# Kernel optimization log

Hardware: AMD Instinct MI355X
Metric: run time of the kernel (lower is better)

The kernel has to match this reference:

```python
import jax, jax.numpy as jnp
import numpy as np

L, B, T, C, H, FC = 8, 4, 2048, 1024, 16, 4
HD = C // H  # head dim = 64
DFF = FC * C  # 4096


def _layernorm(x, g, b, eps=1e-5):
    mu = jnp.mean(x, axis=-1, keepdims=True)
    var = jnp.mean(jnp.square(x - mu), axis=-1, keepdims=True)
    return (x - mu) * jax.lax.rsqrt(var + eps) * g + b


def setup_inputs() -> dict:
    key = jax.random.key(0)
    ks = jax.random.split(key, 18)
    s = 0.02
    d = {}
    d["x"] = jax.random.normal(ks[0], (B, T, C), jnp.float32)
    d["ln1_g"] = jnp.ones((L, C), jnp.float32)
    d["ln1_b"] = jnp.zeros((L, C), jnp.float32)
    d["ln2_g"] = jnp.ones((L, C), jnp.float32)
    d["ln2_b"] = jnp.zeros((L, C), jnp.float32)
    d["wq"] = jax.random.normal(ks[1], (L, C, C), jnp.float32) * s
    d["bq"] = jnp.zeros((L, C), jnp.float32)
    d["wk"] = jax.random.normal(ks[2], (L, C, C), jnp.float32) * s
    d["bk"] = jnp.zeros((L, C), jnp.float32)
    d["wv"] = jax.random.normal(ks[3], (L, C, C), jnp.float32) * s
    d["bv"] = jnp.zeros((L, C), jnp.float32)
    d["wo"] = jax.random.normal(ks[4], (L, C, C), jnp.float32) * s
    d["bo"] = jnp.zeros((L, C), jnp.float32)
    d["w1"] = jax.random.normal(ks[5], (L, C, DFF), jnp.float32) * s
    d["b1"] = jnp.zeros((L, DFF), jnp.float32)
    d["w2"] = jax.random.normal(ks[6], (L, DFF, C), jnp.float32) * s
    d["b2"] = jnp.zeros((L, C), jnp.float32)
    return d


def _forward(x, ln1_g, ln1_b, ln2_g, ln2_b, wq, bq, wk, bk, wv, bv, wo, bo, w1, b1, w2, b2):
    mask = jnp.tril(jnp.ones((T, T), dtype=bool))  # causal mask (block_size buffer)
    scale = 1.0 / np.sqrt(HD).astype(np.float32)

    def block(h, p):
        g1, be1, g2, be2, Wq, Bq, Wk, Bk, Wv, Bv, Wo, Bo, W1, B1, W2, B2 = p
        hn = _layernorm(h, g1, be1)
        # heads: [B, H, T, HD]
        q = (hn @ Wq + Bq).reshape(B, T, H, HD).transpose(0, 2, 1, 3)
        k = (hn @ Wk + Bk).reshape(B, T, H, HD).transpose(0, 2, 1, 3)
        v = (hn @ Wv + Bv).reshape(B, T, H, HD).transpose(0, 2, 1, 3)
        att = jnp.einsum('bhid,bhjd->bhij', q, k) * scale
        att = jnp.where(mask, att, -jnp.inf)
        att = jax.nn.softmax(att, axis=-1)
        y = jnp.einsum('bhij,bhjd->bhid', att, v)
        y = y.transpose(0, 2, 1, 3).reshape(B, T, C) @ Wo + Bo
        h = h + y
        m = _layernorm(h, g2, be2)
        h = h + jax.nn.gelu(m @ W1 + B1, approximate=False) @ W2 + B2
        return h, None

    params = (ln1_g, ln1_b, ln2_g, ln2_b, wq, bq, wk, bk, wv, bv, wo, bo, w1, b1, w2, b2)
    x, _ = jax.lax.scan(block, x, params)
    return x


def reference(x, ln1_g, ln1_b, ln2_g, ln2_b, wq, bq, wk, bk, wv, bv, wo, bo, w1, b1, w2, b2):
    return _forward(x, ln1_g, ln1_b, ln2_g, ln2_b, wq, bq, wk, bk, wv, bv, wo, bo, w1, b1, w2, b2)
```

## Files before the change

kernel.cpp:

```cpp
#include <hip/hip_runtime.h>
#include <hip/hip_bf16.h>

#define LL 8
#define BBx 4
#define TT 2048
#define CC 1024
#define HH 16
#define HDD 64
#define DFFx 4096
#define MMx 8192

typedef __bf16 bf16;
typedef __attribute__((ext_vector_type(8))) __bf16 bf16x8;
typedef __attribute__((ext_vector_type(4))) __bf16 bf16x4;
typedef __attribute__((ext_vector_type(4))) float f32x4;
typedef __attribute__((ext_vector_type(8))) unsigned short u16x8;

#define QSCALE 0.18033688f

__device__ __forceinline__ unsigned short bfbits(float v) {
  return __builtin_bit_cast(unsigned short, (__bf16)v);
}

__device__ __forceinline__ float fexp2(float x) {
#if __has_builtin(__builtin_amdgcn_exp2f)
  return __builtin_amdgcn_exp2f(x);
#else
  float r;
  asm volatile("v_exp_f32 %0, %1\n\ts_nop 0" : "=v"(r) : "v"(x));
  return r;
#endif
}

__device__ __forceinline__ int xcd_swz(int id, int nwg) {
  return (id & 7) * (nwg >> 3) + (id >> 3);
}

#define GLDS(gp, lp) __builtin_amdgcn_global_load_lds( \
    (const __attribute__((address_space(1))) void*)(gp), \
    (__attribute__((address_space(3))) void*)(lp), 16, 0, 0)

__global__ __launch_bounds__(256) void transpose_cast(
    const float* __restrict__ W, bf16* __restrict__ Wt,
    int K, int N, long srcStride, long dstStride)
{
  __shared__ float tile[32][33];
  const float* Wl = W + (size_t)blockIdx.z * srcStride;
  bf16* Wtl = Wt + (size_t)blockIdx.z * dstStride;
  const int n0 = blockIdx.x * 32, k0 = blockIdx.y * 32;
  const int tx = threadIdx.x, ty = threadIdx.y;
#pragma unroll
  for (int i = 0; i < 32; i += 8)
    tile[ty + i][tx] = Wl[(size_t)(k0 + ty + i) * N + n0 + tx];
  __syncthreads();
#pragma unroll
  for (int i = 0; i < 32; i += 8)
    Wtl[(size_t)(n0 + ty + i) * K + k0 + tx] = (bf16)tile[tx][ty + i];
}

__global__ __launch_bounds__(256) void ln_cmb(
    float* __restrict__ h, const float* __restrict__ p0, const float* __restrict__ p1,
    const float* __restrict__ gamma, const float* __restrict__ beta,
    bf16* __restrict__ out)
{
  const int row = blockIdx.x, tid = threadIdx.x;
  const size_t base = (size_t)row * CC + tid * 4;
  float4 v = *(const float4*)(h + base);
  if (p0) {
    const float4 a = *(const float4*)(p0 + base);
    const float4 b = *(const float4*)(p1 + base);
    v.x += a.x + b.x; v.y += a.y + b.y; v.z += a.z + b.z; v.w += a.w + b.w;
    *(float4*)(h + base) = v;
  }
  if (!out) return;
  float s  = v.x + v.y + v.z + v.w;
  float ss = v.x * v.x + v.y * v.y + v.z * v.z + v.w * v.w;
#pragma unroll
  for (int o = 32; o >= 1; o >>= 1) {
    s  += __shfl_xor(s, o);
    ss += __shfl_xor(ss, o);
  }
  __shared__ float rs[4], rss[4];
  const int w = tid >> 6, l = tid & 63;
  if (l == 0) { rs[w] = s; rss[w] = ss; }
  __syncthreads();
  s  = rs[0] + rs[1] + rs[2] + rs[3];
  ss = rss[0] + rss[1] + rss[2] + rss[3];
  const float mu = s * (1.f / CC);
  const float rstd = rsqrtf(ss * (1.f / CC) - mu * mu + 1e-5f);
  const float4 g  = *(const float4*)(gamma + tid * 4);
  const float4 be = *(const float4*)(beta + tid * 4);
  bf16x4 o4;
  o4[0] = (bf16)((v.x - mu) * rstd * g.x + be.x);
  o4[1] = (bf16)((v.y - mu) * rstd * g.y + be.y);
  o4[2] = (bf16)((v.z - mu) * rstd * g.z + be.z);
  o4[3] = (bf16)((v.w - mu) * rstd * g.w + be.w);
  *(bf16x4*)(out + (size_t)row * CC + tid * 4) = o4;
}

template<int EPI>
__global__ __launch_bounds__(256, 4) void gemm128(
    const bf16* __restrict__ A, const bf16* __restrict__ Bt,
    const float* __restrict__ bias0, const float* __restrict__ bias1,
    const float* __restrict__ bias2,
    bf16* __restrict__ o0, bf16* __restrict__ o1, bf16* __restrict__ o2,
    float* __restrict__ p0, float* __restrict__ p1,
    int M, int N, int K, int lda)
{
  __shared__ __align__(16) bf16 sA[128 * 64];
  __shared__ __align__(16) bf16 sB[128 * 64];
  const int nx = N >> 7;
  int wk = xcd_swz((int)blockIdx.x, (int)gridDim.x);
  int koff = 0;
  float* part = p0;
  bool addb = true;
  if constexpr (EPI == 1) {
    const int tiles = nx * (M >> 7);
    const int ks = wk / tiles;
    wk -= ks * tiles;
    koff = ks * K;
    addb = (ks == 0);
    part = ks ? p1 : p0;
  }
  const int m0 = (wk / nx) * 128;
  const int n0 = (wk % nx) * 128;
  const int tid = threadIdx.x;
  const int w = tid >> 6, l = tid & 63;
  const int wr = w >> 1, wc = w & 1;
  const int lr = l & 15, lk = l >> 4;

  f32x4 acc[4][4] = {};
  const int NT = K >> 6;

  for (int kt = 0; kt < NT; ++kt) {
#pragma unroll
    for (int i = 0; i < 4; ++i) {
      const int e = (tid << 4) + (i << 12);
      const int ro = e >> 7, co = (e & 127) >> 1;
      GLDS(A + (size_t)(m0 + ro) * lda + kt * 64 + koff + co, sA + (e >> 1));
      GLDS(Bt + (size_t)(n0 + ro) * lda + kt * 64 + koff + co, sB + (e >> 1));
    }
    __syncthreads();
#pragma unroll
    for (int kk = 0; kk < 2; ++kk) {
      bf16x8 af[4], bfr[4];
#pragma unroll
      for (int i = 0; i < 4; ++i)
        af[i] = *(const bf16x8*)&sA[(wr * 64 + i * 16 + lr) * 64 + kk * 32 + lk * 8];
#pragma unroll
      for (int j = 0; j < 4; ++j)
        bfr[j] = *(const bf16x8*)&sB[(wc * 64 + j * 16 + lr) * 64 + kk * 32 + lk * 8];
#pragma unroll
      for (int i = 0; i < 4; ++i)
#pragma unroll
        for (int j = 0; j < 4; ++j)
          acc[i][j] = __builtin_amdgcn_mfma_f32_16x16x32_bf16(af[i], bfr[j], acc[i][j], 0, 0, 0);
    }
    __syncthreads();
  }

  if constexpr (EPI == 0) {
    const int seg = n0 >> 10;
    const float* bp = (seg == 0) ? bias0 : (seg == 1 ? bias1 : bias2);
    if (seg < 2) {
      const float qs = (seg == 0) ? QSCALE : 1.0f;
      float bv4[4];
#pragma unroll
      for (int j = 0; j < 4; ++j) bv4[j] = bp[(n0 + wc * 64 + j * 16 + lr) & 1023];
      const int hh = ((n0 + wc * 64) & 1023) >> 6;
      bf16* dst = (seg == 0) ? o0 : o1;
#pragma unroll
      for (int i = 0; i < 4; ++i) {
        const int mrow = m0 + wr * 64 + i * 16 + lk * 4;
        const int bidx = mrow >> 11, t = mrow & 2047;
#pragma unroll
        for (int r = 0; r < 4; ++r) {
          bf16* rowp = dst + (((size_t)(bidx * HH + hh)) * TT + t + r) * HDD;
#pragma unroll
          for (int j = 0; j < 4; ++j)
            rowp[j * 16 + lr] = (bf16)((acc[i][j][r] + bv4[j]) * qs);
        }
      }
    } else {
      char* scb = (w < 2) ? ((char*)sA + w * 8192) : ((char*)sB + (w - 2) * 8192);
#pragma unroll
      for (int j = 0; j < 4; ++j) {
        const int dl = j * 16 + lr;
        const float bv = bias2[(n0 + wc * 64 + dl) & 1023];
#pragma unroll
        for (int i = 0; i < 4; ++i) {
          ushort4 pk;
          pk.x = bfbits(acc[i][j][0] + bv);
          pk.y = bfbits(acc[i][j][1] + bv);
          pk.z = bfbits(acc[i][j][2] + bv);
          pk.w = bfbits(acc[i][j][3] + bv);
          *(ushort4*)(scb + dl * 128 + (((i * 16 + lk * 4) * 2) ^ ((dl & 7) << 4))) = pk;
        }
      }
      asm volatile("s_waitcnt lgkmcnt(0)" ::: "memory");
      const int hh = ((n0 + wc * 64) & 1023) >> 6;
      const int bidx = (m0 + wr * 64) >> 11;
      const int tb = (m0 + wr * 64) & 2047;
      const int c = l & 7;
#pragma unroll
      for (int g = 0; g < 8; ++g) {
        const int dl = g * 8 + (l >> 3);
        u16x8 val = *(const u16x8*)(scb + dl * 128 + ((c * 16) ^ ((dl & 7) << 4)));
        *(u16x8*)&o2[(((size_t)(bidx * HH + hh)) * HDD + dl) * TT + tb + c * 8] = val;
      }
    }
  } else if constexpr (EPI == 1) {
    float bv4[4];
#pragma unroll
    for (int j = 0; j < 4; ++j)
      bv4[j] = addb ? bias0[n0 + wc * 64 + j * 16 + lr] : 0.f;
#pragma unroll
    for (int i = 0; i < 4; ++i) {
      const int mrow = m0 + wr * 64 + i * 16 + lk * 4;
#pragma unroll
      for (int r = 0; r < 4; ++r) {
        float* rowp = part + (size_t)(mrow + r) * N + n0 + wc * 64;
#pragma unroll
        for (int j = 0; j < 4; ++j)
          rowp[j * 16 + lr] = acc[i][j][r] + bv4[j];
      }
    }
  } else {
    float bv4[4];
#pragma unroll
    for (int j = 0; j < 4; ++j) bv4[j] = bias0[n0 + wc * 64 + j * 16 + lr];
#pragma unroll
    for (int i = 0; i < 4; ++i) {
      const int mrow = m0 + wr * 64 + i * 16 + lk * 4;
#pragma unroll
      for (int r = 0; r < 4; ++r) {
        bf16* rowp = o0 + (size_t)(mrow + r) * N + n0 + wc * 64;
#pragma unroll
        for (int j = 0; j < 4; ++j) {
          const float x = acc[i][j][r] + bv4[j];
          rowp[j * 16 + lr] = (bf16)(0.5f * x * (1.f + erff(x * 0.70710678f)));
        }
      }
    }
  }
  (void)M;
}

__global__ __launch_bounds__(256) void attn_fwd(
    const bf16* __restrict__ Q, const bf16* __restrict__ Kk,
    const bf16* __restrict__ Vt, bf16* __restrict__ O)
{
  const int wk = xcd_swz((int)blockIdx.x, (int)gridDim.x);
  const int bh = wk >> 3;
  const int xt = wk & 7;
  const int tid = threadIdx.x;
  const int w = tid >> 6, l = tid & 63;
  const int lr = l & 15, lk = l >> 4;
  const int bidx = bh >> 4, hh = bh & 15;

  const bf16* Qp = Q  + (size_t)bh * (TT * HDD);
  const bf16* Kp = Kk + (size_t)bh * (TT * HDD);
  const bf16* Vp = Vt + (size_t)bh * (HDD * TT);

  __shared__ __align__(16) bf16 sK[64 * 64];
  __shared__ __align__(16) bf16 sV[64 * 64];
  __shared__ __align__(16) bf16 sP[4][16 * 64];
  bf16* sPw = &sP[w][0];

  const int swz = (lr & 7) * 8;
  const int srow = tid >> 3;
  const int scol = (((tid & 7) ^ (srow & 7)) << 3);
  const int sdst = tid << 3;

  for (int half = 0; half < 2; ++half) {
    const int qtile = (half == 0) ? xt : (15 - xt);
    const int q0 = qtile * 128;

    bf16x8 qf[2][2];
#pragma unroll
    for (int qi = 0; qi < 2; ++qi)
#pragma unroll
      for (int dk = 0; dk < 2; ++dk)
        qf[qi][dk] = *(const bf16x8*)&Qp[(size_t)(q0 + w * 32 + qi * 16 + lr) * HDD + dk * 32 + lk * 8];

    f32x4 accO[2][4] = {};
    float mrun[2] = {-__builtin_inff(), -__builtin_inff()};
    float lrun[2] = {0.f, 0.f};
    const int wqmax = q0 + w * 32 + 31;
    const int kvend = q0 + 128;

    for (int kv = 0; kv < kvend; kv += 64) {
      __syncthreads();
#pragma unroll
      for (int i = 0; i < 2; ++i) {
        GLDS(Kp + (size_t)(kv + srow + i * 32) * HDD + scol, sK + sdst + i * 2048);
        GLDS(Vp + (size_t)(srow + i * 32) * TT + kv + scol, sV + sdst + i * 2048);
      }
      __syncthreads();

      if (kv <= wqmax) {
#pragma unroll
        for (int qi = 0; qi < 2; ++qi) {
          f32x4 st[4];
#pragma unroll
          for (int kt = 0; kt < 4; ++kt) {
            f32x4 z = {0.f, 0.f, 0.f, 0.f};
#pragma unroll
            for (int dk = 0; dk < 2; ++dk) {
              bf16x8 kf = *(const bf16x8*)&sK[(kt * 16 + lr) * 64 + ((dk * 32 + lk * 8) ^ swz)];
              z = __builtin_amdgcn_mfma_f32_16x16x32_bf16(kf, qf[qi][dk], z, 0, 0, 0);
            }
            st[kt] = z;
          }
          const int qabs_base = q0 + w * 32 + qi * 16;
          float pm = -__builtin_inff();
          if (kv + 63 > qabs_base) {
            const int qabs = qabs_base + lr;
#pragma unroll
            for (int kt = 0; kt < 4; ++kt)
#pragma unroll
              for (int r = 0; r < 4; ++r) {
                const int kvabs = kv + kt * 16 + lk * 4 + r;
                float val = (kvabs > qabs) ? -__builtin_inff() : st[kt][r];
                st[kt][r] = val;
                pm = fmaxf(pm, val);
              }
          } else {
#pragma unroll
            for (int kt = 0; kt < 4; ++kt)
#pragma unroll
              for (int r = 0; r < 4; ++r) pm = fmaxf(pm, st[kt][r]);
          }
          pm = fmaxf(pm, __shfl_xor(pm, 16));
          pm = fmaxf(pm, __shfl_xor(pm, 32));
          const float mnew = fmaxf(mrun[qi], pm);
          const float alpha = fexp2(mrun[qi] - mnew);
          mrun[qi] = mnew;
          float psum = 0.f;
#pragma unroll
          for (int kt = 0; kt < 4; ++kt) {
            const float p0v = fexp2(st[kt][0] - mnew);
            const float p1v = fexp2(st[kt][1] - mnew);
            const float p2v = fexp2(st[kt][2] - mnew);
            const float p3v = fexp2(st[kt][3] - mnew);
            psum += p0v + p1v + p2v + p3v;
            ushort4 pk;
            pk.x = bfbits(p0v); pk.y = bfbits(p1v); pk.z = bfbits(p2v); pk.w = bfbits(p3v);
            *(ushort4*)&sPw[lr * 64 + ((kt * 16 + lk * 4) ^ swz)] = pk;
          }
          psum += __shfl_xor(psum, 16);
          psum += __shfl_xor(psum, 32);
          lrun[qi] = lrun[qi] * alpha + psum;
          f32x4 al4;
#pragma unroll
          for (int r = 0; r < 4; ++r) al4[r] = __shfl(alpha, lk * 4 + r);
#pragma unroll
          for (int dj = 0; dj < 4; ++dj) accO[qi][dj] *= al4;
#pragma unroll
          for (int kt2 = 0; kt2 < 2; ++kt2) {
            bf16x8 pf = *(const bf16x8*)&sPw[lr * 64 + ((kt2 * 32 + lk * 8) ^ swz)];
#pragma unroll
            for (int dj = 0; dj < 4; ++dj) {
              bf16x8 vf = *(const bf16x8*)&sV[(dj * 16 + lr) * 64 + ((kt2 * 32 + lk * 8) ^ swz)];
              accO[qi][dj] = __builtin_amdgcn_mfma_f32_16x16x32_bf16(pf, vf, accO[qi][dj], 0, 0, 0);
            }
          }
        }
      }
    }

#pragma unroll
    for (int qi = 0; qi < 2; ++qi) {
      const float linv = 1.f / lrun[qi];
      f32x4 li4;
#pragma unroll
      for (int r = 0; r < 4; ++r) li4[r] = __shfl(linv, lk * 4 + r);
      const int tbase = q0 + w * 32 + qi * 16 + lk * 4;
#pragma unroll
      for (int dj = 0; dj < 4; ++dj)
#pragma unroll
        for (int r = 0; r < 4; ++r)
          O[((size_t)bidx * TT + tbase + r) * CC + hh * 64 + dj * 16 + lr] =
              (bf16)(accO[qi][dj][r] * li4[r]);
    }
  }
}

extern "C" void kernel_launch(void* const* d_in, const int* in_sizes, int n_in,
                              void* d_out, int out_size, void* d_ws, size_t ws_size,
                              hipStream_t stream)
{
  const float* x    = (const float*)d_in[0];
  const float* ln1g = (const float*)d_in[1];
  const float* ln1b = (const float*)d_in[2];
  const float* ln2g = (const float*)d_in[3];
  const float* ln2b = (const float*)d_in[4];
  const float* wq   = (const float*)d_in[5];
  const float* bq   = (const float*)d_in[6];
  const float* wk   = (const float*)d_in[7];
  const float* bk   = (const float*)d_in[8];
  const float* wv   = (const float*)d_in[9];
  const float* bvv  = (const float*)d_in[10];
  const float* wo   = (const float*)d_in[11];
  const float* bo   = (const float*)d_in[12];
  const float* w1   = (const float*)d_in[13];
  const float* b1   = (const float*)d_in[14];
  const float* w2   = (const float*)d_in[15];
  const float* b2   = (const float*)d_in[16];

  float* h = (float*)d_out;
  bf16* ws = (bf16*)d_ws;
  bf16* wqkvT = ws;
  bf16* woT   = wqkvT + (size_t)LL * 3 * CC * CC;
  bf16* w1T   = woT + (size_t)LL * CC * CC;
  bf16* w2T   = w1T + (size_t)LL * CC * DFFx;
  bf16* hn    = w2T + (size_t)LL * CC * DFFx;
  bf16* qb    = hn + (size_t)MMx * CC;
  bf16* kb    = qb + (size_t)MMx * CC;
  bf16* vt    = kb + (size_t)MMx * CC;
  bf16* ab    = vt + (size_t)MMx * CC;
  bf16* mid   = ab + (size_t)MMx * CC;

  float* pw0 = (float*)mid;
  float* pw1 = (float*)mid + (size_t)MMx * CC;
  float* pm0 = (float*)qb;
  float* pm1 = (float*)vt;

  hipMemcpyAsync(h, x, (size_t)MMx * CC * sizeof(float), hipMemcpyDeviceToDevice, stream);

  dim3 tb(32, 8);
  transpose_cast<<<dim3(CC / 32, CC / 32, LL), tb, 0, stream>>>(wq, wqkvT, CC, CC, (long)CC * CC, (long)3 * CC * CC);
  transpose_cast<<<dim3(CC / 32, CC / 32, LL), tb, 0, stream>>>(wk, wqkvT + CC * CC, CC, CC, (long)CC * CC, (long)3 * CC * CC);
  transpose_cast<<<dim3(CC / 32, CC / 32, LL), tb, 0, stream>>>(wv, wqkvT + 2 * CC * CC, CC, CC, (long)CC * CC, (long)3 * CC * CC);
  transpose_cast<<<dim3(CC / 32, CC / 32, LL), tb, 0, stream>>>(wo, woT, CC, CC, (long)CC * CC, (long)CC * CC);
  transpose_cast<<<dim3(DFFx / 32, CC / 32, LL), tb, 0, stream>>>(w1, w1T, CC, DFFx, (long)CC * DFFx, (long)CC * DFFx);
  transpose_cast<<<dim3(CC / 32, DFFx / 32, LL), tb, 0, stream>>>(w2, w2T, DFFx, CC, (long)CC * DFFx, (long)CC * DFFx);

  for (int li = 0; li < LL; ++li) {
    if (li == 0)
      ln_cmb<<<MMx, 256, 0, stream>>>(h, nullptr, nullptr, ln1g, ln1b, hn);
    else
      ln_cmb<<<MMx, 256, 0, stream>>>(h, pm0, pm1, ln1g + li * CC, ln1b + li * CC, hn);
    gemm128<0><<<(3 * CC / 128) * (MMx / 128), 256, 0, stream>>>(
        hn, wqkvT + (size_t)li * 3 * CC * CC, bq + li * CC, bk + li * CC, bvv + li * CC,
        qb, kb, vt, nullptr, nullptr, MMx, 3 * CC, CC, CC);
    attn_fwd<<<8 * BBx * HH, 256, 0, stream>>>(qb, kb, vt, ab);
    gemm128<1><<<2 * (CC / 128) * (MMx / 128), 256, 0, stream>>>(
        ab, woT + (size_t)li * CC * CC, bo + li * CC, nullptr, nullptr,
        nullptr, nullptr, nullptr, pw0, pw1, MMx, CC, CC / 2, CC);
    ln_cmb<<<MMx, 256, 0, stream>>>(h, pw0, pw1, ln2g + li * CC, ln2b + li * CC, hn);
    gemm128<2><<<(DFFx / 128) * (MMx / 128), 256, 0, stream>>>(
        hn, w1T + (size_t)li * CC * DFFx, b1 + li * DFFx, nullptr, nullptr,
        mid, nullptr, nullptr, nullptr, nullptr, MMx, DFFx, CC, CC);
    gemm128<1><<<2 * (CC / 128) * (MMx / 128), 256, 0, stream>>>(
        mid, w2T + (size_t)li * CC * DFFx, b2 + li * CC, nullptr, nullptr,
        nullptr, nullptr, nullptr, pm0, pm1, MMx, CC, DFFx / 2, DFFx);
  }
  ln_cmb<<<MMx, 256, 0, stream>>>(h, pm0, pm1, nullptr, nullptr, nullptr);
  (void)in_sizes; (void)n_in; (void)out_size; (void)ws_size;
}
```

Baseline: 3.272 ms.

## Add 256x256 double-buffered GEMM kernel for QKV, FFN1 and FFN2

Adds a gemm256 kernel with 512 threads, 256x256 output tiles, double-buffered LDS staging interleaved with MFMA phases, swizzled LDS layout, and setprio around MFMA bursts. QKV, FFN-up and FFN-down GEMMs switch to it, while gemm128 is trimmed to the split-K fp32 epilogue used for the output projection. The larger tiles are meant to raise arithmetic intensity and hide global-load latency. In exchange the kernel uses more LDS and registers (lower occupancy) and launches fewer blocks, which can leave CUs underused for the N=1024 split-K GEMM.

```diff
diff --git a/kernel.cpp b/kernel.cpp
--- a/kernel.cpp
+++ b/kernel.cpp
@@ -101,9 +101,7 @@
 template<int EPI>
 __global__ __launch_bounds__(256, 4) void gemm128(
     const bf16* __restrict__ A, const bf16* __restrict__ Bt,
-    const float* __restrict__ bias0, const float* __restrict__ bias1,
-    const float* __restrict__ bias2,
-    bf16* __restrict__ o0, bf16* __restrict__ o1, bf16* __restrict__ o2,
+    const float* __restrict__ bias0,
     float* __restrict__ p0, float* __restrict__ p1,
     int M, int N, int K, int lda)
 {
@@ -158,6 +156,120 @@
     }
     __syncthreads();
   }
+  float bv4[4];
+#pragma unroll
+  for (int j = 0; j < 4; ++j)
+    bv4[j] = addb ? bias0[n0 + wc * 64 + j * 16 + lr] : 0.f;
+#pragma unroll
+  for (int i = 0; i < 4; ++i) {
+    const int mrow = m0 + wr * 64 + i * 16 + lk * 4;
+#pragma unroll
+    for (int r = 0; r < 4; ++r) {
+      float* rowp = part + (size_t)(mrow + r) * N + n0 + wc * 64;
+#pragma unroll
+      for (int j = 0; j < 4; ++j)
+        rowp[j * 16 + lr] = acc[i][j][r] + bv4[j];
+    }
+  }
+  (void)M;
+}
+
+template<int EPI>
+__global__ __launch_bounds__(512, 2) void gemm256(
+    const bf16* __restrict__ A, const bf16* __restrict__ Bt,
+    const float* __restrict__ bias0, const float* __restrict__ bias1,
+    const float* __restrict__ bias2,
+    bf16* __restrict__ o0, bf16* __restrict__ o1, bf16* __restrict__ o2,
+    float* __restrict__ p0w, float* __restrict__ p1w,
+    int M, int N, int K, int lda)
+{
+  __shared__ __align__(16) bf16 sA[2][256 * 64];
+  __shared__ __align__(16) bf16 sB[2][256 * 64];
+  const int nx = N >> 8;
+  int wk = xcd_swz((int)blockIdx.x, (int)gridDim.x);
+  int koff = 0;
+  float* part = p0w;
+  bool addb = true;
+  if constexpr (EPI == 1) {
+    const int tiles = nx * (M >> 8);
+    const int ks = wk / tiles;
+    wk -= ks * tiles;
+    koff = ks * K;
+    addb = (ks == 0);
+    part = ks ? p1w : p0w;
+  }
+  const int m0 = (wk / nx) * 256;
+  const int n0 = (wk % nx) * 256;
+  const int tid = threadIdx.x;
+  const int w = tid >> 6, l = tid & 63;
+  const int wm = w >> 2, wn = w & 3;
+  const int lr = l & 15, lk = l >> 4;
+  const int sr = tid >> 3, ss = tid & 7;
+  const int gcs = (ss ^ (sr & 7)) << 3;
+
+  f32x4 acc[8][4] = {};
+  const int NT = K >> 6;
+
+  auto stageq = [&](int b, int kt, int q) {
+    const int gc = gcs + kt * 64 + koff;
+    const int rb = (q & 1) * 128;
+    if (q < 2) {
+#pragma unroll
+      for (int i = 0; i < 2; ++i) {
+        const int r = rb + sr + i * 64;
+        GLDS(A + (size_t)(m0 + r) * lda + gc, &sA[b][r * 64 + ss * 8]);
+      }
+    } else {
+#pragma unroll
+      for (int i = 0; i < 2; ++i) {
+        const int r = rb + sr + i * 64;
+        GLDS(Bt + (size_t)(n0 + r) * lda + gc, &sB[b][r * 64 + ss * 8]);
+      }
+    }
+  };
+
+  stageq(0, 0, 0); stageq(0, 0, 1); stageq(0, 0, 2); stageq(0, 0, 3);
+  asm volatile("s_waitcnt vmcnt(2)" ::: "memory");
+  __builtin_amdgcn_s_barrier();
+
+  bf16x8 af[8], bf2[2];
+  for (int t = 0; t < NT; ++t) {
+    const int cur = t & 1, nxt = cur ^ 1;
+    const bool pre = (t + 1 < NT);
+#pragma unroll
+    for (int ph = 0; ph < 4; ++ph) {
+      const int kk = ph >> 1, nh = ph & 1;
+      if (nh == 0) {
+#pragma unroll
+        for (int m = 0; m < 8; ++m) {
+          const int row = wm * 128 + m * 16 + lr;
+          af[m] = *(const bf16x8*)&sA[cur][row * 64 + (((kk * 4 + lk) ^ (row & 7)) << 3)];
+        }
+      }
+#pragma unroll
+      for (int j2 = 0; j2 < 2; ++j2) {
+        const int row = nh * 128 + wn * 32 + j2 * 16 + lr;
+        bf2[j2] = *(const bf16x8*)&sB[cur][row * 64 + (((kk * 4 + lk) ^ (row & 7)) << 3)];
+      }
+      if (pre) stageq(nxt, t + 1, ph);
+      if (ph == 0 || ph == 3) {
+        if (pre) asm volatile("s_waitcnt vmcnt(2)" ::: "memory");
+        else     asm volatile("s_waitcnt vmcnt(0)" ::: "memory");
+      }
+      __builtin_amdgcn_s_barrier();
+      asm volatile("s_waitcnt lgkmcnt(0)" ::: "memory");
+      __builtin_amdgcn_sched_barrier(0);
+      __builtin_amdgcn_s_setprio(1);
+#pragma unroll
+      for (int m = 0; m < 8; ++m)
+#pragma unroll
+        for (int j2 = 0; j2 < 2; ++j2)
+          acc[m][nh * 2 + j2] = __builtin_amdgcn_mfma_f32_16x16x32_bf16(
+              af[m], bf2[j2], acc[m][nh * 2 + j2], 0, 0, 0);
+      __builtin_amdgcn_s_setprio(0);
+      __builtin_amdgcn_s_barrier();
+    }
+  }
 
   if constexpr (EPI == 0) {
     const int seg = n0 >> 10;
@@ -165,81 +277,93 @@
     if (seg < 2) {
       const float qs = (seg == 0) ? QSCALE : 1.0f;
       float bv4[4];
-#pragma unroll
-      for (int j = 0; j < 4; ++j) bv4[j] = bp[(n0 + wc * 64 + j * 16 + lr) & 1023];
-      const int hh = ((n0 + wc * 64) & 1023) >> 6;
+      int hh4[4], dd4[4];
+#pragma unroll
+      for (int jj = 0; jj < 4; ++jj) {
+        const int c1024 = (n0 + (jj >> 1) * 128 + wn * 32 + (jj & 1) * 16 + lr) & 1023;
+        bv4[jj] = bp[c1024];
+        hh4[jj] = c1024 >> 6;
+        dd4[jj] = c1024 & 63;
+      }
       bf16* dst = (seg == 0) ? o0 : o1;
 #pragma unroll
-      for (int i = 0; i < 4; ++i) {
-        const int mrow = m0 + wr * 64 + i * 16 + lk * 4;
+      for (int m = 0; m < 8; ++m) {
+        const int mrow = m0 + wm * 128 + m * 16 + lk * 4;
         const int bidx = mrow >> 11, t = mrow & 2047;
 #pragma unroll
         for (int r = 0; r < 4; ++r) {
-          bf16* rowp = dst + (((size_t)(bidx * HH + hh)) * TT + t + r) * HDD;
-#pragma unroll
-          for (int j = 0; j < 4; ++j)
-            rowp[j * 16 + lr] = (bf16)((acc[i][j][r] + bv4[j]) * qs);
+#pragma unroll
+          for (int jj = 0; jj < 4; ++jj)
+            dst[(((size_t)(bidx * HH + hh4[jj])) * TT + t + r) * HDD + dd4[jj]] =
+                (bf16)((acc[m][jj][r] + bv4[jj]) * qs);
         }
       }
     } else {
-      char* scb = (w < 2) ? ((char*)sA + w * 8192) : ((char*)sB + (w - 2) * 8192);
-#pragma unroll
-      for (int j = 0; j < 4; ++j) {
-        const int dl = j * 16 + lr;
-        const float bv = bias2[(n0 + wc * 64 + dl) & 1023];
-#pragma unroll
-        for (int i = 0; i < 4; ++i) {
+      char* scb = (char*)((w < 4) ? (&sA[0][0] + w * 8192) : (&sB[0][0] + (w - 4) * 8192));
+#pragma unroll
+      for (int jj = 0; jj < 4; ++jj) {
+        const int dloc = (jj >> 1) * 32 + (jj & 1) * 16 + lr;
+        const int dglob = (n0 & 1023) + (jj >> 1) * 128 + wn * 32 + (jj & 1) * 16 + lr;
+        const float bv = bias2[dglob];
+#pragma unroll
+        for (int m = 0; m < 8; ++m) {
           ushort4 pk;
-          pk.x = bfbits(acc[i][j][0] + bv);
-          pk.y = bfbits(acc[i][j][1] + bv);
-          pk.z = bfbits(acc[i][j][2] + bv);
-          pk.w = bfbits(acc[i][j][3] + bv);
-          *(ushort4*)(scb + dl * 128 + (((i * 16 + lk * 4) * 2) ^ ((dl & 7) << 4))) = pk;
+          pk.x = bfbits(acc[m][jj][0] + bv);
+          pk.y = bfbits(acc[m][jj][1] + bv);
+          pk.z = bfbits(acc[m][jj][2] + bv);
+          pk.w = bfbits(acc[m][jj][3] + bv);
+          *(ushort4*)(scb + dloc * 256 + (((m * 16 + lk * 4) * 2) ^ ((dloc & 7) << 4))) = pk;
         }
       }
       asm volatile("s_waitcnt lgkmcnt(0)" ::: "memory");
-      const int hh = ((n0 + wc * 64) & 1023) >> 6;
-      const int bidx = (m0 + wr * 64) >> 11;
-      const int tb = (m0 + wr * 64) & 2047;
-      const int c = l & 7;
-#pragma unroll
-      for (int g = 0; g < 8; ++g) {
-        const int dl = g * 8 + (l >> 3);
-        u16x8 val = *(const u16x8*)(scb + dl * 128 + ((c * 16) ^ ((dl & 7) << 4)));
-        *(u16x8*)&o2[(((size_t)(bidx * HH + hh)) * HDD + dl) * TT + tb + c * 8] = val;
+      const int bidx = m0 >> 11;
+      const int tb = (m0 & 2047) + wm * 128;
+      const int c = l & 15;
+#pragma unroll
+      for (int g = 0; g < 16; ++g) {
+        const int dloc = g * 4 + lk;
+        const int dglob = (n0 & 1023) + (dloc >> 5) * 128 + wn * 32 + (dloc & 31);
+        const int hh = dglob >> 6, dd = dglob & 63;
+        u16x8 val = *(const u16x8*)(scb + dloc * 256 + ((c * 16) ^ ((dloc & 7) << 4)));
+        *(u16x8*)&o2[(((size_t)(bidx * HH + hh)) * HDD + dd) * TT + tb + c * 8] = val;
       }
     }
   } else if constexpr (EPI == 1) {
     float bv4[4];
 #pragma unroll
-    for (int j = 0; j < 4; ++j)
-      bv4[j] = addb ? bias0[n0 + wc * 64 + j * 16 + lr] : 0.f;
-#pragma unroll
-    for (int i = 0; i < 4; ++i) {
-      const int mrow = m0 + wr * 64 + i * 16 + lk * 4;
+    for (int jj = 0; jj < 4; ++jj)
+      bv4[jj] = addb ? bias0[n0 + (jj >> 1) * 128 + wn * 32 + (jj & 1) * 16 + lr] : 0.f;
+#pragma unroll
+    for (int m = 0; m < 8; ++m) {
+      const int mrow = m0 + wm * 128 + m * 16 + lk * 4;
 #pragma unroll
       for (int r = 0; r < 4; ++r) {
-        float* rowp = part + (size_t)(mrow + r) * N + n0 + wc * 64;
-#pragma unroll
-        for (int j = 0; j < 4; ++j)
-          rowp[j * 16 + lr] = acc[i][j][r] + bv4[j];
+        float* rowp = part + (size_t)(mrow + r) * N + n0 + wn * 32;
+        rowp[lr]        = acc[m][0][r] + bv4[0];
+        rowp[16 + lr]   = acc[m][1][r] + bv4[1];
+        rowp[128 + lr]  = acc[m][2][r] + bv4[2];
+        rowp[144 + lr]  = acc[m][3][r] + bv4[3];
       }
     }
   } else {
     float bv4[4];
 #pragma unroll
-    for (int j = 0; j < 4; ++j) bv4[j] = bias0[n0 + wc * 64 + j * 16 + lr];
-#pragma unroll
-    for (int i = 0; i < 4; ++i) {
-      const int mrow = m0 + wr * 64 + i * 16 + lk * 4;
+    for (int jj = 0; jj < 4; ++jj)
+      bv4[jj] = bias0[n0 + (jj >> 1) * 128 + wn * 32 + (jj & 1) * 16 + lr];
+#pragma unroll
+    for (int m = 0; m < 8; ++m) {
+      const int mrow = m0 + wm * 128 + m * 16 + lk * 4;
 #pragma unroll
       for (int r = 0; r < 4; ++r) {
-        bf16* rowp = o0 + (size_t)(mrow + r) * N + n0 + wc * 64;
-#pragma unroll
-        for (int j = 0; j < 4; ++j) {
-          const float x = acc[i][j][r] + bv4[j];
-          rowp[j * 16 + lr] = (bf16)(0.5f * x * (1.f + erff(x * 0.70710678f)));
-        }
+        bf16* rowp = o0 + (size_t)(mrow + r) * N + n0 + wn * 32;
+        const float x0 = acc[m][0][r] + bv4[0];
+        const float x1 = acc[m][1][r] + bv4[1];
+        const float x2 = acc[m][2][r] + bv4[2];
+        const float x3 = acc[m][3][r] + bv4[3];
+        rowp[lr]       = (bf16)(0.5f * x0 * (1.f + erff(x0 * 0.70710678f)));
+        rowp[16 + lr]  = (bf16)(0.5f * x1 * (1.f + erff(x1 * 0.70710678f)));
+        rowp[128 + lr] = (bf16)(0.5f * x2 * (1.f + erff(x2 * 0.70710678f)));
+        rowp[144 + lr] = (bf16)(0.5f * x3 * (1.f + erff(x3 * 0.70710678f)));
       }
     }
   }
@@ -441,18 +565,17 @@
       ln_cmb<<<MMx, 256, 0, stream>>>(h, nullptr, nullptr, ln1g, ln1b, hn);
     else
       ln_cmb<<<MMx, 256, 0, stream>>>(h, pm0, pm1, ln1g + li * CC, ln1b + li * CC, hn);
-    gemm128<0><<<(3 * CC / 128) * (MMx / 128), 256, 0, stream>>>(
+    gemm256<0><<<(3 * CC / 256) * (MMx / 256), 512, 0, stream>>>(
         hn, wqkvT + (size_t)li * 3 * CC * CC, bq + li * CC, bk + li * CC, bvv + li * CC,
         qb, kb, vt, nullptr, nullptr, MMx, 3 * CC, CC, CC);
     attn_fwd<<<8 * BBx * HH, 256, 0, stream>>>(qb, kb, vt, ab);
     gemm128<1><<<2 * (CC / 128) * (MMx / 128), 256, 0, stream>>>(
-        ab, woT + (size_t)li * CC * CC, bo + li * CC, nullptr, nullptr,
-        nullptr, nullptr, nullptr, pw0, pw1, MMx, CC, CC / 2, CC);
+        ab, woT + (size_t)li * CC * CC, bo + li * CC, pw0, pw1, MMx, CC, CC / 2, CC);
     ln_cmb<<<MMx, 256, 0, stream>>>(h, pw0, pw1, ln2g + li * CC, ln2b + li * CC, hn);
-    gemm128<2><<<(DFFx / 128) * (MMx / 128), 256, 0, stream>>>(
+    gemm256<2><<<(DFFx / 256) * (MMx / 256), 512, 0, stream>>>(
         hn, w1T + (size_t)li * CC * DFFx, b1 + li * DFFx, nullptr, nullptr,
         mid, nullptr, nullptr, nullptr, nullptr, MMx, DFFx, CC, CC);
-    gemm128<1><<<2 * (CC / 128) * (MMx / 128), 256, 0, stream>>>(
+    gemm256<1><<<2 * (CC / 256) * (MMx / 256), 512, 0, stream>>>(
         mid, w2T + (size_t)li * CC * DFFx, b2 + li * CC, nullptr, nullptr,
         nullptr, nullptr, nullptr, pm0, pm1, MMx, CC, DFFx / 2, DFFx);
   }
```

New measurement: 3.315 ms. About the same (+1.3%).
